# Kernel tuning notes

Measured on AMD Instinct MI355X. Metric: run time of the kernel, lower is better.

The kernel has to match this reference:

```python
import jax, jax.numpy as jnp
import numpy as np

D = 768  # in_channels == out_channels (forced by residual + shared LayerNorm)
B, S = 8, 2048


def setup_inputs() -> dict:
    key = jax.random.key(0)
    ks = jax.random.split(key, 5)
    x = jax.random.normal(ks[0], (B, S, D), dtype=jnp.float32)
    # LayerNorm params
    ln_g = jnp.ones((D,), dtype=jnp.float32)
    ln_b = jnp.zeros((D,), dtype=jnp.float32)
    # Q/K linear params (torch Linear: y = x @ W.T + b)
    scale = 1.0 / np.sqrt(D)
    Wq = jax.random.uniform(ks[1], (D, D), jnp.float32, -scale, scale)
    bq = jax.random.uniform(ks[2], (D,), jnp.float32, -scale, scale)
    Wk = jax.random.uniform(ks[3], (D, D), jnp.float32, -scale, scale)
    bk = jax.random.uniform(ks[4], (D,), jnp.float32, -scale, scale)
    return {"x": x, "ln_g": ln_g, "ln_b": ln_b, "Wq": Wq, "bq": bq, "Wk": Wk, "bk": bk}


def _layernorm(x, g, b, eps=1e-5):
    mu = jnp.mean(x, axis=-1, keepdims=True)
    var = jnp.mean(jnp.square(x - mu), axis=-1, keepdims=True)
    return (x - mu) * jax.lax.rsqrt(var + eps) * g + b


def reference(x, ln_g, ln_b, Wq, bq, Wk, bk):
    origin = x
    xn = _layernorm(x, ln_g, ln_b)
    Q = xn @ Wq.T + bq  # [B,S,D]
    K = xn @ Wk.T + bk  # [B,S,D]
    scores = jnp.einsum('bsd,btd->bst', Q, K) / jnp.sqrt(jnp.asarray(D, x.dtype))
    attn = jax.nn.softmax(scores, axis=-1)  # [B,S,S]
    out = jnp.einsum('bst,btd->bsd', attn, origin) + origin
    # note: original then computes relu(layernorm(out)) but returns `out` (dead code)
    return out
```

## Files before the change

### kernel.cpp

```cpp
#include <hip/hip_runtime.h>

typedef __bf16 bf16;
typedef __bf16 v8bf __attribute__((ext_vector_type(8)));
typedef __bf16 v4bf __attribute__((ext_vector_type(4)));
typedef float  v4f  __attribute__((ext_vector_type(4)));

__device__ __forceinline__ void gload_lds16(const void* g, void* l) {
    __builtin_amdgcn_global_load_lds(
        (const __attribute__((address_space(1))) void*)g,
        (__attribute__((address_space(3))) void*)l, 16, 0, 0);
}

#define MFMA16(a, b, c) __builtin_amdgcn_mfma_f32_16x16x32_bf16((a), (b), (c), 0, 0, 0)

__global__ __launch_bounds__(256)
void ln_cast(const float* __restrict__ x, const float* __restrict__ g,
             const float* __restrict__ b, bf16* __restrict__ xn,
             bf16* __restrict__ xv, float* __restrict__ L)
{
    const long row = blockIdx.x;
    const float* xr = x + row * 768;
    const int tid = threadIdx.x;
    const int wave = tid >> 6, lane = tid & 63;

    if (row < 64) L[row * 256 + tid] = 0.0f;

    float a0 = xr[tid], a1 = xr[tid + 256], a2 = xr[tid + 512];
    float s = a0 + a1 + a2;
    #pragma unroll
    for (int off = 32; off; off >>= 1) s += __shfl_xor(s, off);
    __shared__ float sh[4], sh2[4];
    if (!lane) sh[wave] = s;
    __syncthreads();
    const float mu = (sh[0] + sh[1] + sh[2] + sh[3]) * (1.0f / 768.0f);

    float d0 = a0 - mu, d1 = a1 - mu, d2 = a2 - mu;
    float ss = d0 * d0 + d1 * d1 + d2 * d2;
    #pragma unroll
    for (int off = 32; off; off >>= 1) ss += __shfl_xor(ss, off);
    if (!lane) sh2[wave] = ss;
    __syncthreads();
    const float var = (sh2[0] + sh2[1] + sh2[2] + sh2[3]) * (1.0f / 768.0f);
    const float rstd = rsqrtf(var + 1e-5f);

    bf16* xnr = xn + row * 768;
    bf16* xvr = xv + row * 768;
    xnr[tid]       = (bf16)(d0 * rstd * g[tid]       + b[tid]);
    xnr[tid + 256] = (bf16)(d1 * rstd * g[tid + 256] + b[tid + 256]);
    xnr[tid + 512] = (bf16)(d2 * rstd * g[tid + 512] + b[tid + 512]);
    xvr[tid]       = (bf16)a0;
    xvr[tid + 256] = (bf16)a1;
    xvr[tid + 512] = (bf16)a2;
}

__global__ __launch_bounds__(256)
void cvt_w(const float* __restrict__ Wq, const float* __restrict__ Wk,
           bf16* __restrict__ Wcat)
{
    const int z = blockIdx.y;
    const float* src = z ? Wk : Wq;
    bf16* dst = Wcat + (long)z * 768 * 768;
    const int i = (blockIdx.x * 256 + threadIdx.x) * 4;
    const float4 v = *(const float4*)(src + i);
    v4bf o = {(bf16)v.x, (bf16)v.y, (bf16)v.z, (bf16)v.w};
    *(v4bf*)(dst + i) = o;
}

__global__ __launch_bounds__(256)
void transpose_bf(const bf16* __restrict__ in, bf16* __restrict__ outT)
{
    __shared__ __attribute__((aligned(16))) bf16 tile[64 * 64];
    const int t0 = blockIdx.x * 64, d0 = blockIdx.y * 64;
    in   += (long)blockIdx.z * 2048 * 768;
    outT += (long)blockIdx.z * 768 * 2048;
    const int tid = threadIdx.x;

    #pragma unroll
    for (int it = 0; it < 2; ++it) {
        const int lin = it * 256 + tid;
        const int r = lin >> 3;
        const int g = lin & 7;
        const int pg = g ^ (r & 7) ^ ((r >> 3) & 7);
        v8bf v = *(const v8bf*)(in + (long)(t0 + r) * 768 + d0 + g * 8);
        *(v8bf*)(tile + r * 64 + pg * 8) = v;
    }
    __syncthreads();
    #pragma unroll
    for (int it = 0; it < 2; ++it) {
        const int lin = it * 256 + tid;
        const int dd = lin >> 3;
        const int tb = lin & 7;
        v8bf o;
        #pragma unroll
        for (int j = 0; j < 8; ++j) {
            const int t = tb * 8 + j;
            const int pg = (dd >> 3) ^ (t & 7) ^ ((t >> 3) & 7);
            o[j] = tile[t * 64 + pg * 8 + (dd & 7)];
        }
        *(v8bf*)(outT + (long)(d0 + dd) * 2048 + t0 + tb * 8) = o;
    }
}

__global__ __launch_bounds__(512, 2)
void gemm_qk(const bf16* __restrict__ A, const bf16* __restrict__ W,
             const float* __restrict__ bq, const float* __restrict__ bk,
             float qscale, bf16* __restrict__ Qb, bf16* __restrict__ Kb)
{
    __shared__ __attribute__((aligned(16))) bf16 lds[2][32768];

    const int bx = blockIdx.x;
    const int wg = (bx & 7) * 64 + (bx >> 3);
    const int m0 = (wg >> 2) * 128;
    const int n0 = (wg & 3) * 384;

    const bf16* Ag = A + (long)m0 * 768;
    const bf16* Bg = W + (long)n0 * 768;

    const int tid = threadIdx.x, wv = tid >> 6, lane = tid & 63;
    const int wr = wv >> 2, wc = wv & 3;
    const int lr = lane & 15, lq = lane >> 4;

    auto stA = [&](int bi, int h, int kk) {
        const int lin = wv * 64 + lane;
        const int r = lin >> 3, ck = (lin & 7) ^ (r & 7);
        gload_lds16(Ag + (long)(h * 64 + r) * 768 + kk + ck * 8,
                    (char*)lds + bi * 65536 + h * 8192 + lin * 16);
    };
    auto stB = [&](int bi, int h, int p, int kk) {
        const int lin = (wv * 3 + p) * 64 + lane;
        const int r = lin >> 3, ck = (lin & 7) ^ (r & 7);
        gload_lds16(Bg + (long)(h * 192 + r) * 768 + kk + ck * 8,
                    (char*)lds + bi * 65536 + 16384 + h * 24576 + lin * 16);
    };

    v8bf aS1[2][2], aS2[2][2], aS3[2][2], bS4[3][2], bS5[3][2];
    v4f acc[2][2][2][3] = {};

    auto rdA = [&](v8bf (&d)[2][2], const bf16* Ls, int mh) {
        #pragma unroll
        for (int i = 0; i < 2; ++i) {
            const int r = mh * 64 + wr * 32 + i * 16 + lr;
            #pragma unroll
            for (int s = 0; s < 2; ++s)
                d[i][s] = *(const v8bf*)(Ls + r * 64 + (((s * 4 + lq) ^ (r & 7)) << 3));
        }
    };
    auto rdB = [&](v8bf (&d)[3][2], const bf16* Ls, int nh) {
        #pragma unroll
        for (int n = 0; n < 3; ++n) {
            const int r = nh * 192 + wc * 48 + n * 16 + lr;
            #pragma unroll
            for (int s = 0; s < 2; ++s)
                d[n][s] = *(const v8bf*)(Ls + 8192 + r * 64 + (((s * 4 + lq) ^ (r & 7)) << 3));
        }
    };
    auto mm = [&](v8bf (&a)[2][2], v8bf (&b)[3][2], v4f (&ac)[2][3]) {
        __builtin_amdgcn_s_setprio(1);
        #pragma unroll
        for (int s = 0; s < 2; ++s)
            #pragma unroll
            for (int i = 0; i < 2; ++i)
                #pragma unroll
                for (int n = 0; n < 3; ++n)
                    ac[i][n] = MFMA16(a[i][s], b[n][s], ac[i][n]);
        __builtin_amdgcn_s_setprio(0);
    };

    const int NT = 12;
    stA(0, 0, 0); stB(0, 0, 0, 0); stB(0, 0, 1, 0); stB(0, 0, 2, 0);
    stA(0, 1, 0); stB(0, 1, 0, 0); stB(0, 1, 1, 0); stB(0, 1, 2, 0);
    asm volatile("s_waitcnt vmcnt(3)" ::: "memory");
    __builtin_amdgcn_s_barrier();
    rdA(aS1, lds[0], 0); rdB(bS4, lds[0], 0);

    for (int t = 0; t < NT; ++t) {
        const int cur = t & 1, nxt = cur ^ 1;
        const int kk2 = (t + 1 < NT ? t + 1 : t) * 64;
        const bf16* Ls = lds[cur];
        const bf16* Ln = lds[nxt];

        rdA(aS2, Ls, 1);
        stA(nxt, 0, kk2);
        mm(aS1, bS4, acc[0][0]);
        asm volatile("s_waitcnt vmcnt(1)" ::: "memory");
        __builtin_amdgcn_s_barrier();

        rdB(bS5, Ls, 1);
        stB(nxt, 0, 0, kk2); stB(nxt, 0, 1, kk2); stB(nxt, 0, 2, kk2);
        mm(aS2, bS4, acc[1][0]);
        __builtin_amdgcn_s_barrier();

        rdA(aS3, Ls, 0);
        stA(nxt, 1, kk2);
        mm(aS2, bS5, acc[1][1]);
        asm volatile("s_waitcnt vmcnt(1)" ::: "memory");
        __builtin_amdgcn_s_barrier();

        rdA(aS1, Ln, 0); rdB(bS4, Ln, 0);
        stB(nxt, 1, 0, kk2); stB(nxt, 1, 1, kk2); stB(nxt, 1, 2, kk2);
        mm(aS3, bS5, acc[0][1]);
        asm volatile("s_waitcnt vmcnt(3)" ::: "memory");
        __builtin_amdgcn_s_barrier();
    }
    asm volatile("s_waitcnt vmcnt(0)" ::: "memory");

    const bool isQ = (n0 < 768);
    const float* bias = isQ ? bq : bk;
    const float sc = isQ ? qscale : 1.0f;
    bf16* C = isQ ? Qb : Kb;
    const int c0 = isQ ? n0 : n0 - 768;

    #pragma unroll
    for (int mh = 0; mh < 2; ++mh)
    #pragma unroll
    for (int i = 0; i < 2; ++i) {
        #pragma unroll
        for (int rr = 0; rr < 4; ++rr) {
            const int row = m0 + mh * 64 + wr * 32 + i * 16 + lq * 4 + rr;
            #pragma unroll
            for (int nh = 0; nh < 2; ++nh)
                #pragma unroll
                for (int n = 0; n < 3; ++n) {
                    const int col = c0 + nh * 192 + wc * 48 + n * 16 + lr;
                    C[(long)row * 768 + col] = (bf16)((acc[mh][nh][i][n][rr] + bias[col]) * sc);
                }
        }
    }
}

__global__ __launch_bounds__(512, 2)
void gemm_scores(const bf16* __restrict__ Q, const bf16* __restrict__ K,
                 bf16* __restrict__ E, float* __restrict__ L)
{
    __shared__ __attribute__((aligned(16))) bf16 lds[2][32768];

    const int bx = blockIdx.x;
    const int batch = bx & 7, j = bx >> 3;
    const int m0 = (j >> 3) * 256, n0 = (j & 7) * 256;

    const bf16* Ag = Q + (long)batch * 2048 * 768 + (long)m0 * 768;
    const bf16* Bg = K + (long)batch * 2048 * 768 + (long)n0 * 768;
    bf16* C = E + (long)batch * 2048 * 2048;
    float* Lb = L + (long)batch * 2048;

    const int tid = threadIdx.x, wv = tid >> 6, lane = tid & 63;
    const int wr = wv >> 2, wc = wv & 3;
    const int lr = lane & 15, lq = lane >> 4;

    auto stA = [&](int bi, int h, int p, int kk) {
        const int lin = (wv * 2 + p) * 64 + lane;
        const int r = lin >> 3, ck = (lin & 7) ^ (r & 7);
        gload_lds16(Ag + (long)(h * 128 + r) * 768 + kk + ck * 8,
                    (char*)lds + bi * 65536 + h * 16384 + lin * 16);
    };
    auto stB = [&](int bi, int h, int p, int kk) {
        const int lin = (wv * 2 + p) * 64 + lane;
        const int r = lin >> 3, ck = (lin & 7) ^ (r & 7);
        gload_lds16(Bg + (long)(h * 128 + r) * 768 + kk + ck * 8,
                    (char*)lds + bi * 65536 + 32768 + h * 16384 + lin * 16);
    };

    v8bf aS1[4][2], aS2[4][2], aS3[4][2], bS4[2][2], bS5[2][2];
    v4f acc[2][2][4][2] = {};

    auto rdA = [&](v8bf (&d)[4][2], const bf16* Ls, int mh) {
        #pragma unroll
        for (int i = 0; i < 4; ++i) {
            const int r = mh * 128 + wr * 64 + i * 16 + lr;
            #pragma unroll
            for (int s = 0; s < 2; ++s)
                d[i][s] = *(const v8bf*)(Ls + r * 64 + (((s * 4 + lq) ^ (r & 7)) << 3));
        }
    };
    auto rdB = [&](v8bf (&d)[2][2], const bf16* Ls, int nh) {
        #pragma unroll
        for (int n = 0; n < 2; ++n) {
            const int r = nh * 128 + wc * 32 + n * 16 + lr;
            #pragma unroll
            for (int s = 0; s < 2; ++s)
                d[n][s] = *(const v8bf*)(Ls + 16384 + r * 64 + (((s * 4 + lq) ^ (r & 7)) << 3));
        }
    };
    auto mm = [&](v8bf (&a)[4][2], v8bf (&b)[2][2], v4f (&ac)[4][2]) {
        __builtin_amdgcn_s_setprio(1);
        #pragma unroll
        for (int s = 0; s < 2; ++s)
            #pragma unroll
            for (int i = 0; i < 4; ++i)
                #pragma unroll
                for (int n = 0; n < 2; ++n)
                    ac[i][n] = MFMA16(a[i][s], b[n][s], ac[i][n]);
        __builtin_amdgcn_s_setprio(0);
    };

    const int NT = 12;
    stA(0, 0, 0, 0); stA(0, 0, 1, 0); stB(0, 0, 0, 0); stB(0, 0, 1, 0);
    stA(0, 1, 0, 0); stA(0, 1, 1, 0); stB(0, 1, 0, 0); stB(0, 1, 1, 0);
    asm volatile("s_waitcnt vmcnt(2)" ::: "memory");
    __builtin_amdgcn_s_barrier();
    rdA(aS1, lds[0], 0); rdB(bS4, lds[0], 0);

    for (int t = 0; t < NT; ++t) {
        const int cur = t & 1, nxt = cur ^ 1;
        const int kk2 = (t + 1 < NT ? t + 1 : t) * 64;
        const bf16* Ls = lds[cur];
        const bf16* Ln = lds[nxt];

        rdA(aS2, Ls, 1);
        stA(nxt, 0, 0, kk2); stA(nxt, 0, 1, kk2);
        mm(aS1, bS4, acc[0][0]);
        asm volatile("s_waitcnt vmcnt(2)" ::: "memory");
        __builtin_amdgcn_s_barrier();

        rdB(bS5, Ls, 1);
        stB(nxt, 0, 0, kk2); stB(nxt, 0, 1, kk2);
        mm(aS2, bS4, acc[1][0]);
        asm volatile("s_waitcnt vmcnt(2)" ::: "memory");
        __builtin_amdgcn_s_barrier();

        rdA(aS3, Ls, 0);
        stA(nxt, 1, 0, kk2); stA(nxt, 1, 1, kk2);
        mm(aS2, bS5, acc[1][1]);
        asm volatile("s_waitcnt vmcnt(2)" ::: "memory");
        __builtin_amdgcn_s_barrier();

        rdA(aS1, Ln, 0); rdB(bS4, Ln, 0);
        stB(nxt, 1, 0, kk2); stB(nxt, 1, 1, kk2);
        mm(aS3, bS5, acc[0][1]);
        asm volatile("s_waitcnt vmcnt(2)" ::: "memory");
        __builtin_amdgcn_s_barrier();
    }
    asm volatile("s_waitcnt vmcnt(0)" ::: "memory");

    #pragma unroll
    for (int mh = 0; mh < 2; ++mh)
    #pragma unroll
    for (int i = 0; i < 4; ++i) {
        #pragma unroll
        for (int rr = 0; rr < 4; ++rr) {
            const int row = m0 + mh * 128 + wr * 64 + i * 16 + lq * 4 + rr;
            float e[4], rs = 0.f;
            #pragma unroll
            for (int nh = 0; nh < 2; ++nh)
                #pragma unroll
                for (int n = 0; n < 2; ++n) {
                    e[nh * 2 + n] = __expf(acc[mh][nh][i][n][rr]);
                    rs += e[nh * 2 + n];
                }
            #pragma unroll
            for (int off = 1; off < 16; off <<= 1) rs += __shfl_xor(rs, off);
            if (lr == 0) atomicAdd(&Lb[row], rs);
            #pragma unroll
            for (int nh = 0; nh < 2; ++nh)
                #pragma unroll
                for (int n = 0; n < 2; ++n) {
                    const int col = n0 + nh * 128 + wc * 32 + n * 16 + lr;
                    C[(long)row * 2048 + col] = (bf16)e[nh * 2 + n];
                }
        }
    }
}

__global__ __launch_bounds__(512, 2)
void gemm_pv(const bf16* __restrict__ P, const bf16* __restrict__ VT,
             const float* __restrict__ L, const float* __restrict__ Xres,
             float* __restrict__ Out)
{
    __shared__ __attribute__((aligned(16))) bf16 lds[2][32768];

    const int bx = blockIdx.x;
    const int batch = bx & 7, j = bx >> 3;
    const int m0 = (j >> 1) * 128;
    const int n0 = (j & 1) * 384;

    const bf16* Ag = P  + (long)batch * 2048 * 2048 + (long)m0 * 2048;
    const bf16* Bg = VT + (long)batch * 768 * 2048  + (long)n0 * 2048;
    const float* Lb = L + (long)batch * 2048;
    const float* Xr = Xres + (long)batch * 2048 * 768;
    float* O = Out + (long)batch * 2048 * 768;

    const int tid = threadIdx.x, wv = tid >> 6, lane = tid & 63;
    const int wr = wv >> 2, wc = wv & 3;
    const int lr = lane & 15, lq = lane >> 4;

    auto stA = [&](int bi, int h, int kk) {
        const int lin = wv * 64 + lane;
        const int r = lin >> 3, ck = (lin & 7) ^ (r & 7);
        gload_lds16(Ag + (long)(h * 64 + r) * 2048 + kk + ck * 8,
                    (char*)lds + bi * 65536 + h * 8192 + lin * 16);
    };
    auto stB = [&](int bi, int h, int p, int kk) {
        const int lin = (wv * 3 + p) * 64 + lane;
        const int r = lin >> 3, ck = (lin & 7) ^ (r & 7);
        gload_lds16(Bg + (long)(h * 192 + r) * 2048 + kk + ck * 8,
                    (char*)lds + bi * 65536 + 16384 + h * 24576 + lin * 16);
    };

    v8bf aS1[2][2], aS2[2][2], aS3[2][2], bS4[3][2], bS5[3][2];
    v4f acc[2][2][2][3] = {};

    auto rdA = [&](v8bf (&d)[2][2], const bf16* Ls, int mh) {
        #pragma unroll
        for (int i = 0; i < 2; ++i) {
            const int r = mh * 64 + wr * 32 + i * 16 + lr;
            #pragma unroll
            for (int s = 0; s < 2; ++s)
                d[i][s] = *(const v8bf*)(Ls + r * 64 + (((s * 4 + lq) ^ (r & 7)) << 3));
        }
    };
    auto rdB = [&](v8bf (&d)[3][2], const bf16* Ls, int nh) {
        #pragma unroll
        for (int n = 0; n < 3; ++n) {
            const int r = nh * 192 + wc * 48 + n * 16 + lr;
            #pragma unroll
            for (int s = 0; s < 2; ++s)
                d[n][s] = *(const v8bf*)(Ls + 8192 + r * 64 + (((s * 4 + lq) ^ (r & 7)) << 3));
        }
    };
    auto mm = [&](v8bf (&a)[2][2], v8bf (&b)[3][2], v4f (&ac)[2][3]) {
        __builtin_amdgcn_s_setprio(1);
        #pragma unroll
        for (int s = 0; s < 2; ++s)
            #pragma unroll
            for (int i = 0; i < 2; ++i)
                #pragma unroll
                for (int n = 0; n < 3; ++n)
                    ac[i][n] = MFMA16(a[i][s], b[n][s], ac[i][n]);
        __builtin_amdgcn_s_setprio(0);
    };

    const int NT = 32;
    stA(0, 0, 0); stB(0, 0, 0, 0); stB(0, 0, 1, 0); stB(0, 0, 2, 0);
    stA(0, 1, 0); stB(0, 1, 0, 0); stB(0, 1, 1, 0); stB(0, 1, 2, 0);
    asm volatile("s_waitcnt vmcnt(3)" ::: "memory");
    __builtin_amdgcn_s_barrier();
    rdA(aS1, lds[0], 0); rdB(bS4, lds[0], 0);

    for (int t = 0; t < NT; ++t) {
        const int cur = t & 1, nxt = cur ^ 1;
        const int kk2 = (t + 1 < NT ? t + 1 : t) * 64;
        const bf16* Ls = lds[cur];
        const bf16* Ln = lds[nxt];

        rdA(aS2, Ls, 1);
        stA(nxt, 0, kk2);
        mm(aS1, bS4, acc[0][0]);
        asm volatile("s_waitcnt vmcnt(1)" ::: "memory");
        __builtin_amdgcn_s_barrier();

        rdB(bS5, Ls, 1);
        stB(nxt, 0, 0, kk2); stB(nxt, 0, 1, kk2); stB(nxt, 0, 2, kk2);
        mm(aS2, bS4, acc[1][0]);
        __builtin_amdgcn_s_barrier();

        rdA(aS3, Ls, 0);
        stA(nxt, 1, kk2);
        mm(aS2, bS5, acc[1][1]);
        asm volatile("s_waitcnt vmcnt(1)" ::: "memory");
        __builtin_amdgcn_s_barrier();

        rdA(aS1, Ln, 0); rdB(bS4, Ln, 0);
        stB(nxt, 1, 0, kk2); stB(nxt, 1, 1, kk2); stB(nxt, 1, 2, kk2);
        mm(aS3, bS5, acc[0][1]);
        asm volatile("s_waitcnt vmcnt(3)" ::: "memory");
        __builtin_amdgcn_s_barrier();
    }
    asm volatile("s_waitcnt vmcnt(0)" ::: "memory");

    #pragma unroll
    for (int mh = 0; mh < 2; ++mh)
    #pragma unroll
    for (int i = 0; i < 2; ++i) {
        #pragma unroll
        for (int rr = 0; rr < 4; ++rr) {
            const int row = m0 + mh * 64 + wr * 32 + i * 16 + lq * 4 + rr;
            const float invL = 1.0f / Lb[row];
            #pragma unroll
            for (int nh = 0; nh < 2; ++nh)
                #pragma unroll
                for (int n = 0; n < 3; ++n) {
                    const int col = n0 + nh * 192 + wc * 48 + n * 16 + lr;
                    const long idx = (long)row * 768 + col;
                    O[idx] = acc[mh][nh][i][n][rr] * invL + Xr[idx];
                }
        }
    }
}

extern "C" void kernel_launch(void* const* d_in, const int* in_sizes, int n_in,
                              void* d_out, int out_size, void* d_ws, size_t ws_size,
                              hipStream_t stream)
{
    const float* x    = (const float*)d_in[0];
    const float* ln_g = (const float*)d_in[1];
    const float* ln_b = (const float*)d_in[2];
    const float* Wq   = (const float*)d_in[3];
    const float* bq   = (const float*)d_in[4];
    const float* Wk   = (const float*)d_in[5];
    const float* bk   = (const float*)d_in[6];
    float* out = (float*)d_out;

    const long R = 8L * 2048;
    char* ws = (char*)d_ws;
    size_t off = 0;
    auto take = [&](size_t bytes) -> char* {
        char* p = ws + off;
        off += (bytes + 255) & ~(size_t)255;
        return p;
    };
    bf16*  xn   = (bf16*)take(R * 768 * 2);
    bf16*  xv   = (bf16*)take(R * 768 * 2);
    bf16*  Qb   = (bf16*)take(R * 768 * 2);
    bf16*  Kb   = (bf16*)take(R * 768 * 2);
    bf16*  Wcat = (bf16*)take(1536L * 768 * 2);
    float* Lrow = (float*)take(R * 4);
    bf16*  Sc   = (bf16*)take(8L * 2048 * 2048 * 2);

    ln_cast<<<R, 256, 0, stream>>>(x, ln_g, ln_b, xn, xv, Lrow);
    cvt_w<<<dim3(576, 2), 256, 0, stream>>>(Wq, Wk, Wcat);

    const float qscale = 0.036084391824351615f;
    gemm_qk<<<512, 512, 0, stream>>>(xn, Wcat, bq, bk, qscale, Qb, Kb);

    bf16* xvT = xn;
    transpose_bf<<<dim3(32, 12, 8), 256, 0, stream>>>(xv, xvT);

    gemm_scores<<<512, 512, 0, stream>>>(Qb, Kb, Sc, Lrow);
    gemm_pv<<<256, 512, 0, stream>>>(Sc, xvT, Lrow, x, out);
}
```

Measured before the change: 369.7 us.

## Shrink scores GEMM tile to 128x256 and double grid with reworked pipeline

The QK^T scores kernel moves from 256x256 to 128x256 output tiles, doubling the grid to 1024 blocks and cutting shared memory to 96KB. The pipeline is rewritten to handle two k-steps per loop iteration with fixed double-buffer pointers and a register ping-pong between A0/A1 and B0/B1. Smaller tiles lower register and LDS pressure, which can raise occupancy and give more blocks for the CUs, at the cost of less operand reuse per block and more K-tile reloads.

```diff
diff --git a/kernel.cpp b/kernel.cpp
--- a/kernel.cpp
+++ b/kernel.cpp
@@ -232,11 +232,11 @@
 void gemm_scores(const bf16* __restrict__ Q, const bf16* __restrict__ K,
                  bf16* __restrict__ E, float* __restrict__ L)
 {
-    __shared__ __attribute__((aligned(16))) bf16 lds[2][32768];
+    __shared__ __attribute__((aligned(16))) bf16 lds[2][24576];
 
     const int bx = blockIdx.x;
     const int batch = bx & 7, j = bx >> 3;
-    const int m0 = (j >> 3) * 256, n0 = (j & 7) * 256;
+    const int m0 = (j >> 3) * 128, n0 = (j & 7) * 256;
 
     const bf16* Ag = Q + (long)batch * 2048 * 768 + (long)m0 * 768;
     const bf16* Bg = K + (long)batch * 2048 * 768 + (long)n0 * 768;
@@ -247,46 +247,48 @@
     const int wr = wv >> 2, wc = wv & 3;
     const int lr = lane & 15, lq = lane >> 4;
 
-    auto stA = [&](int bi, int h, int p, int kk) {
-        const int lin = (wv * 2 + p) * 64 + lane;
+    auto stA = [&](int bi, int h, int kk) {
+        const int lin = wv * 64 + lane;
         const int r = lin >> 3, ck = (lin & 7) ^ (r & 7);
-        gload_lds16(Ag + (long)(h * 128 + r) * 768 + kk + ck * 8,
-                    (char*)lds + bi * 65536 + h * 16384 + lin * 16);
+        gload_lds16(Ag + (long)(h * 64 + r) * 768 + kk + ck * 8,
+                    (char*)lds + bi * 49152 + h * 8192 + lin * 16);
     };
     auto stB = [&](int bi, int h, int p, int kk) {
         const int lin = (wv * 2 + p) * 64 + lane;
         const int r = lin >> 3, ck = (lin & 7) ^ (r & 7);
         gload_lds16(Bg + (long)(h * 128 + r) * 768 + kk + ck * 8,
-                    (char*)lds + bi * 65536 + 32768 + h * 16384 + lin * 16);
-    };
-
-    v8bf aS1[4][2], aS2[4][2], aS3[4][2], bS4[2][2], bS5[2][2];
-    v4f acc[2][2][4][2] = {};
-
-    auto rdA = [&](v8bf (&d)[4][2], const bf16* Ls, int mh) {
-        #pragma unroll
-        for (int i = 0; i < 4; ++i) {
-            const int r = mh * 128 + wr * 64 + i * 16 + lr;
+                    (char*)lds + bi * 49152 + 16384 + h * 16384 + lin * 16);
+    };
+
+    v8bf A0[2][2], A1[2][2], B0[2][2], B1[2][2];
+    v4f acc[2][2][2][2] = {};
+
+    auto rdA = [&](v8bf (&d)[2][2], const bf16* Ls, int mh) {
+        #pragma unroll
+        for (int i = 0; i < 2; ++i) {
+            const int r = wr * 32 + i * 16 + lr;
             #pragma unroll
             for (int s = 0; s < 2; ++s)
-                d[i][s] = *(const v8bf*)(Ls + r * 64 + (((s * 4 + lq) ^ (r & 7)) << 3));
+                d[i][s] = *(const v8bf*)(Ls + mh * 4096 + r * 64 +
+                                         (((s * 4 + lq) ^ (r & 7)) << 3));
         }
     };
     auto rdB = [&](v8bf (&d)[2][2], const bf16* Ls, int nh) {
         #pragma unroll
         for (int n = 0; n < 2; ++n) {
-            const int r = nh * 128 + wc * 32 + n * 16 + lr;
+            const int c = wc * 32 + n * 16 + lr;
             #pragma unroll
             for (int s = 0; s < 2; ++s)
-                d[n][s] = *(const v8bf*)(Ls + 16384 + r * 64 + (((s * 4 + lq) ^ (r & 7)) << 3));
-        }
-    };
-    auto mm = [&](v8bf (&a)[4][2], v8bf (&b)[2][2], v4f (&ac)[4][2]) {
+                d[n][s] = *(const v8bf*)(Ls + 8192 + nh * 8192 + c * 64 +
+                                         (((s * 4 + lq) ^ (c & 7)) << 3));
+        }
+    };
+    auto mm = [&](v8bf (&a)[2][2], v8bf (&b)[2][2], v4f (&ac)[2][2]) {
         __builtin_amdgcn_s_setprio(1);
         #pragma unroll
         for (int s = 0; s < 2; ++s)
             #pragma unroll
-            for (int i = 0; i < 4; ++i)
+            for (int i = 0; i < 2; ++i)
                 #pragma unroll
                 for (int n = 0; n < 2; ++n)
                     ac[i][n] = MFMA16(a[i][s], b[n][s], ac[i][n]);
@@ -294,51 +296,72 @@
     };
 
     const int NT = 12;
-    stA(0, 0, 0, 0); stA(0, 0, 1, 0); stB(0, 0, 0, 0); stB(0, 0, 1, 0);
-    stA(0, 1, 0, 0); stA(0, 1, 1, 0); stB(0, 1, 0, 0); stB(0, 1, 1, 0);
+    stA(0, 0, 0); stB(0, 0, 0, 0); stB(0, 0, 1, 0);
+    stA(0, 1, 0); stB(0, 1, 0, 0); stB(0, 1, 1, 0);
     asm volatile("s_waitcnt vmcnt(2)" ::: "memory");
     __builtin_amdgcn_s_barrier();
-    rdA(aS1, lds[0], 0); rdB(bS4, lds[0], 0);
-
-    for (int t = 0; t < NT; ++t) {
-        const int cur = t & 1, nxt = cur ^ 1;
-        const int kk2 = (t + 1 < NT ? t + 1 : t) * 64;
-        const bf16* Ls = lds[cur];
-        const bf16* Ln = lds[nxt];
-
-        rdA(aS2, Ls, 1);
-        stA(nxt, 0, 0, kk2); stA(nxt, 0, 1, kk2);
-        mm(aS1, bS4, acc[0][0]);
+    rdA(A0, lds[0], 0); rdB(B0, lds[0], 0);
+
+    #pragma unroll 1
+    for (int t = 0; t < NT; t += 2) {
+        const int kk1 = (t + 1) * 64;
+        const int kk2 = (t + 2 < NT ? t + 2 : NT - 1) * 64;
+        const bf16* Lc = lds[0];
+        const bf16* Ln = lds[1];
+
+        rdA(A1, Lc, 1);
+        stA(1, 0, kk1);
+        mm(A0, B0, acc[0][0]);
+        asm volatile("s_waitcnt vmcnt(1)" ::: "memory");
+        __builtin_amdgcn_s_barrier();
+
+        rdB(B1, Lc, 1);
+        stB(1, 0, 0, kk1); stB(1, 0, 1, kk1);
+        mm(A1, B0, acc[1][0]);
+        __builtin_amdgcn_s_barrier();
+
+        stA(1, 1, kk1);
+        mm(A1, B1, acc[1][1]);
+        asm volatile("s_waitcnt vmcnt(1)" ::: "memory");
+        __builtin_amdgcn_s_barrier();
+
+        rdA(A1, Ln, 0); rdB(B0, Ln, 0);
+        stB(1, 1, 0, kk1); stB(1, 1, 1, kk1);
+        mm(A0, B1, acc[0][1]);
         asm volatile("s_waitcnt vmcnt(2)" ::: "memory");
         __builtin_amdgcn_s_barrier();
 
-        rdB(bS5, Ls, 1);
-        stB(nxt, 0, 0, kk2); stB(nxt, 0, 1, kk2);
-        mm(aS2, bS4, acc[1][0]);
+        rdA(A0, Ln, 1);
+        stA(0, 0, kk2);
+        mm(A1, B0, acc[0][0]);
+        asm volatile("s_waitcnt vmcnt(1)" ::: "memory");
+        __builtin_amdgcn_s_barrier();
+
+        rdB(B1, Ln, 1);
+        stB(0, 0, 0, kk2); stB(0, 0, 1, kk2);
+        mm(A0, B0, acc[1][0]);
+        __builtin_amdgcn_s_barrier();
+
+        stA(0, 1, kk2);
+        mm(A0, B1, acc[1][1]);
+        asm volatile("s_waitcnt vmcnt(1)" ::: "memory");
+        __builtin_amdgcn_s_barrier();
+
+        rdA(A0, Lc, 0); rdB(B0, Lc, 0);
+        stB(0, 1, 0, kk2); stB(0, 1, 1, kk2);
+        mm(A1, B1, acc[0][1]);
         asm volatile("s_waitcnt vmcnt(2)" ::: "memory");
         __builtin_amdgcn_s_barrier();
-
-        rdA(aS3, Ls, 0);
-        stA(nxt, 1, 0, kk2); stA(nxt, 1, 1, kk2);
-        mm(aS2, bS5, acc[1][1]);
-        asm volatile("s_waitcnt vmcnt(2)" ::: "memory");
-        __builtin_amdgcn_s_barrier();
-
-        rdA(aS1, Ln, 0); rdB(bS4, Ln, 0);
-        stB(nxt, 1, 0, kk2); stB(nxt, 1, 1, kk2);
-        mm(aS3, bS5, acc[0][1]);
-        asm volatile("s_waitcnt vmcnt(2)" ::: "memory");
-        __builtin_amdgcn_s_barrier();
     }
     asm volatile("s_waitcnt vmcnt(0)" ::: "memory");
 
     #pragma unroll
     for (int mh = 0; mh < 2; ++mh)
     #pragma unroll
-    for (int i = 0; i < 4; ++i) {
+    for (int i = 0; i < 2; ++i) {
         #pragma unroll
         for (int rr = 0; rr < 4; ++rr) {
-            const int row = m0 + mh * 128 + wr * 64 + i * 16 + lq * 4 + rr;
+            const int row = m0 + mh * 64 + wr * 32 + i * 16 + lq * 4 + rr;
             float e[4], rs = 0.f;
             #pragma unroll
             for (int nh = 0; nh < 2; ++nh)
@@ -525,6 +548,6 @@
     bf16* xvT = xn;
     transpose_bf<<<dim3(32, 12, 8), 256, 0, stream>>>(xv, xvT);
 
-    gemm_scores<<<512, 512, 0, stream>>>(Qb, Kb, Sc, Lrow);
+    gemm_scores<<<1024, 512, 0, stream>>>(Qb, Kb, Sc, Lrow);
     gemm_pv<<<256, 512, 0, stream>>>(Sc, xvT, Lrow, x, out);
 }
```

Result: faster. 319.4 us (-13.6%).
